# Optimization experiments

Hardware: AMD Instinct MI355X
Metric: run time of the kernel (lower is better)

The kernel has to match this reference:

```python
import jax, jax.numpy as jnp
import numpy as np

N_NODES = 100000


def _sage_conv(x, edge_index, W_l, b_l, W_r):
    # PyG SAGEConv (aggr='mean', root_weight=True):
    #   out = lin_l(mean_{j in N(i)} x_j) + lin_r(x_i)
    src, dst = edge_index[0], edge_index[1]
    msg = x[src]                                            # [E, C] gather
    agg = jax.ops.segment_sum(msg, dst, num_segments=N_NODES)  # [N, C]
    deg = jax.ops.segment_sum(jnp.ones((edge_index.shape[1],), x.dtype), dst,
                              num_segments=N_NODES)
    agg = agg / jnp.maximum(deg, 1.0)[:, None]              # mean aggregation
    return agg @ W_l + b_l + x @ W_r


def setup_inputs() -> dict:
    key = jax.random.key(0)
    ks = jax.random.split(key, 10)
    d, h = 128, 128
    s = 1.0 / np.sqrt(d)
    x = jax.random.normal(ks[0], (N_NODES, d), dtype=jnp.float32)
    edge_index = jax.random.randint(ks[1], (2, 640000), 0, N_NODES, dtype=jnp.int64)
    return {
        "x": x,
        "edge_index": edge_index,
        "W1_l": jax.random.uniform(ks[2], (d, h), jnp.float32, -s, s),
        "b1": jnp.zeros((h,), jnp.float32),
        "W1_r": jax.random.uniform(ks[3], (d, h), jnp.float32, -s, s),
        "W2_l": jax.random.uniform(ks[4], (h, h), jnp.float32, -s, s),
        "b2": jnp.zeros((h,), jnp.float32),
        "W2_r": jax.random.uniform(ks[5], (h, h), jnp.float32, -s, s),
        "W_lin": jax.random.uniform(ks[6], (h, 1), jnp.float32, -s, s),
        "b_lin": jnp.zeros((1,), jnp.float32),
    }


def reference(x, edge_index, W1_l, b1, W1_r, W2_l, b2, W2_r, W_lin, b_lin):
    h = jax.nn.relu(_sage_conv(x, edge_index, W1_l, b1, W1_r))
    h = jax.nn.relu(_sage_conv(h, edge_index, W2_l, b2, W2_r))
    return h @ W_lin + b_lin  # [N, 1]
```

## Files before the change

### kernel.cpp

```cpp
#include <hip/hip_runtime.h>
#include <hip/hip_bf16.h>


#define ND 128
#define KTOT 256
#define CAP 32
#define AGS 136

typedef __bf16 bf16x8 __attribute__((ext_vector_type(8)));
typedef float floatx16 __attribute__((ext_vector_type(16)));

__device__ inline unsigned short f2bf(float f) {
    union { float f; unsigned u; } v; v.f = f;
    unsigned r = v.u + 0x7fffu + ((v.u >> 16) & 1u);
    return (unsigned short)(r >> 16);
}
__device__ inline float bf_lo(unsigned u) { return __uint_as_float(u << 16); }
__device__ inline float bf_hi(unsigned u) { return __uint_as_float(u & 0xffff0000u); }

__device__ inline bf16x8 ldg_bf8(const unsigned short* p, bool ok) {
    int4 v = {0, 0, 0, 0};
    if (ok) v = *(const int4*)p;
    union { int4 i; bf16x8 b; } u; u.i = v;
    return u.b;
}

__global__ void k_prep_all(const float* __restrict__ x, unsigned short* __restrict__ xbf,
                           int nElems,
                           const float* __restrict__ W1l, const float* __restrict__ W1r,
                           unsigned short* __restrict__ Wt1,
                           const float* __restrict__ W2l, const float* __restrict__ W2r,
                           unsigned short* __restrict__ Wt2,
                           const int* __restrict__ esrc_in, const int* __restrict__ edst_in,
                           int* __restrict__ cnt, int* __restrict__ ebuk, int E) {
    const int t = threadIdx.x;
    const int tid = blockIdx.x * 256 + t;

    const int e = blockIdx.x * 128 + t;
    const bool doE = (t < 128) && (e < E);
    int d0 = 0, s0 = 0;
    if (doE) {
        d0 = edst_in[e];
        s0 = esrc_in[e];
    }

    const int i = tid * 8;
    float4 xa, xc;
    const bool doX = (i < nElems);
    if (doX) {
        xa = *(const float4*)(x + i);
        xc = *(const float4*)(x + i + 4);
    }

    int p0 = -1;
    if (doE) p0 = atomicAdd(&cnt[d0], 1);

    if (doX) {
        uint4 r;
        r.x = (unsigned)f2bf(xa.x) | ((unsigned)f2bf(xa.y) << 16);
        r.y = (unsigned)f2bf(xa.z) | ((unsigned)f2bf(xa.w) << 16);
        r.z = (unsigned)f2bf(xc.x) | ((unsigned)f2bf(xc.y) << 16);
        r.w = (unsigned)f2bf(xc.z) | ((unsigned)f2bf(xc.w) << 16);
        *(uint4*)(xbf + i) = r;
    }

    if (tid < 2 * KTOT * ND) {
        const int half = tid >> 15;
        const int idx = tid & 32767;
        const int nn = idx >> 8;
        const int kk = idx & 255;
        const float* Wl = half ? W2l : W1l;
        const float* Wr = half ? W2r : W1r;
        unsigned short* Wt = half ? Wt2 : Wt1;
        float v = (kk < 128) ? Wl[(size_t)kk * ND + nn] : Wr[(size_t)(kk - 128) * ND + nn];
        Wt[(size_t)nn * KTOT + kk] = f2bf(v);
    }

    if (p0 >= 0 && p0 < CAP) ebuk[d0 * CAP + p0] = s0;
}

__device__ __forceinline__ void gather128(const unsigned short* __restrict__ feat,
                                          const int* __restrict__ cnt,
                                          const int* __restrict__ ebuk,
                                          int n, int m0, int t,
                                          unsigned short* Agg) {
    const int l = t & 15;
    const int g = t >> 4;
    for (int p = 0; p < 8; ++p) {
        const int nl = p * 16 + g;
        const int node = m0 + nl;
        int d = 0;
        if (node < n) d = cnt[node];
        const int dd = min(d, CAP);
        const int* lst = ebuk + (size_t)node * CAP;
        float a0 = 0, a1 = 0, a2 = 0, a3 = 0, a4 = 0, a5 = 0, a6 = 0, a7 = 0;
        const int capi = dd - 1;
        for (int j = 0; j < dd; j += 4) {
            int s0 = lst[j];
            int s1 = lst[min(j + 1, capi)];
            int s2 = lst[min(j + 2, capi)];
            int s3 = lst[min(j + 3, capi)];
            uint4 v0 = ((const uint4*)(feat + (size_t)s0 * ND))[l];
            uint4 v1 = ((const uint4*)(feat + (size_t)s1 * ND))[l];
            uint4 v2 = ((const uint4*)(feat + (size_t)s2 * ND))[l];
            uint4 v3 = ((const uint4*)(feat + (size_t)s3 * ND))[l];
            if (j + 1 >= dd) { v1.x = v1.y = v1.z = v1.w = 0u; }
            if (j + 2 >= dd) { v2.x = v2.y = v2.z = v2.w = 0u; }
            if (j + 3 >= dd) { v3.x = v3.y = v3.z = v3.w = 0u; }
            a0 += bf_lo(v0.x) + bf_lo(v1.x) + bf_lo(v2.x) + bf_lo(v3.x);
            a1 += bf_hi(v0.x) + bf_hi(v1.x) + bf_hi(v2.x) + bf_hi(v3.x);
            a2 += bf_lo(v0.y) + bf_lo(v1.y) + bf_lo(v2.y) + bf_lo(v3.y);
            a3 += bf_hi(v0.y) + bf_hi(v1.y) + bf_hi(v2.y) + bf_hi(v3.y);
            a4 += bf_lo(v0.z) + bf_lo(v1.z) + bf_lo(v2.z) + bf_lo(v3.z);
            a5 += bf_hi(v0.z) + bf_hi(v1.z) + bf_hi(v2.z) + bf_hi(v3.z);
            a6 += bf_lo(v0.w) + bf_lo(v1.w) + bf_lo(v2.w) + bf_lo(v3.w);
            a7 += bf_hi(v0.w) + bf_hi(v1.w) + bf_hi(v2.w) + bf_hi(v3.w);
        }
        float inv = 1.0f / (float)max(d, 1);
        uint4 r;
        r.x = (unsigned)f2bf(a0 * inv) | ((unsigned)f2bf(a1 * inv) << 16);
        r.y = (unsigned)f2bf(a2 * inv) | ((unsigned)f2bf(a3 * inv) << 16);
        r.z = (unsigned)f2bf(a4 * inv) | ((unsigned)f2bf(a5 * inv) << 16);
        r.w = (unsigned)f2bf(a6 * inv) | ((unsigned)f2bf(a7 * inv) << 16);
        *(uint4*)&Agg[nl * AGS + l * 8] = r;
    }
}

__launch_bounds__(256, 2)
__global__ void k_layer1_fused(const unsigned short* __restrict__ feat,
                               const unsigned short* __restrict__ Wt,
                               const float* __restrict__ bias,
                               const int* __restrict__ cnt,
                               const int* __restrict__ ebuk,
                               unsigned short* __restrict__ out, int n) {
    __shared__ __align__(16) unsigned short Agg[128 * AGS];
    const int t = threadIdx.x;
    const int m0 = blockIdx.x * 128;

    gather128(feat, cnt, ebuk, n, m0, t, Agg);
    __syncthreads();

    const int wave = t >> 6, lane = t & 63;
    const int l31 = lane & 31, lhalf = lane >> 5;
    const int wm = (wave >> 1) * 64;
    const int wn = (wave & 1) * 64;

    floatx16 acc[2][2];
#pragma unroll
    for (int i = 0; i < 2; ++i)
#pragma unroll
        for (int j = 0; j < 2; ++j) acc[i][j] = (floatx16)0.0f;

#pragma unroll
    for (int kc = 0; kc < 4; ++kc) {
        const int k0 = kc * 32;
        bf16x8 af[2][2], bfr[2][2];
#pragma unroll
        for (int mi = 0; mi < 2; ++mi)
#pragma unroll
            for (int ks = 0; ks < 2; ++ks)
                af[mi][ks] = *(const bf16x8*)&Agg[(wm + mi * 32 + l31) * AGS + k0 + ks * 16 + lhalf * 8];
#pragma unroll
        for (int ni = 0; ni < 2; ++ni)
#pragma unroll
            for (int ks = 0; ks < 2; ++ks)
                bfr[ni][ks] = *(const bf16x8*)(Wt + (size_t)(wn + ni * 32 + l31) * KTOT + k0 + ks * 16 + lhalf * 8);
#pragma unroll
        for (int mi = 0; mi < 2; ++mi)
#pragma unroll
            for (int ni = 0; ni < 2; ++ni) {
                acc[mi][ni] = __builtin_amdgcn_mfma_f32_32x32x16_bf16(af[mi][0], bfr[ni][0], acc[mi][ni], 0, 0, 0);
                acc[mi][ni] = __builtin_amdgcn_mfma_f32_32x32x16_bf16(af[mi][1], bfr[ni][1], acc[mi][ni], 0, 0, 0);
            }
    }

    const int rA0 = m0 + wm + l31;
    const int rA1 = rA0 + 32;
#pragma unroll
    for (int kc = 4; kc < 8; ++kc) {
        const int k0 = kc * 32;
        const int ka = k0 - 128;
        bf16x8 af[2][2], bfr[2][2];
#pragma unroll
        for (int ks = 0; ks < 2; ++ks) {
            af[0][ks] = ldg_bf8(feat + (size_t)rA0 * ND + ka + ks * 16 + lhalf * 8, rA0 < n);
            af[1][ks] = ldg_bf8(feat + (size_t)rA1 * ND + ka + ks * 16 + lhalf * 8, rA1 < n);
        }
#pragma unroll
        for (int ni = 0; ni < 2; ++ni)
#pragma unroll
            for (int ks = 0; ks < 2; ++ks)
                bfr[ni][ks] = *(const bf16x8*)(Wt + (size_t)(wn + ni * 32 + l31) * KTOT + k0 + ks * 16 + lhalf * 8);
#pragma unroll
        for (int mi = 0; mi < 2; ++mi)
#pragma unroll
            for (int ni = 0; ni < 2; ++ni) {
                acc[mi][ni] = __builtin_amdgcn_mfma_f32_32x32x16_bf16(af[mi][0], bfr[ni][0], acc[mi][ni], 0, 0, 0);
                acc[mi][ni] = __builtin_amdgcn_mfma_f32_32x32x16_bf16(af[mi][1], bfr[ni][1], acc[mi][ni], 0, 0, 0);
            }
    }

#pragma unroll
    for (int mi = 0; mi < 2; ++mi)
#pragma unroll
        for (int ni = 0; ni < 2; ++ni) {
            const int c = wn + ni * 32 + l31;
            const float bv = bias[c];
#pragma unroll
            for (int reg = 0; reg < 16; ++reg) {
                const int row = m0 + wm + mi * 32 + lhalf * 4 + (reg & 3) + 8 * (reg >> 2);
                if (row < n) {
                    float v = fmaxf(acc[mi][ni][reg] + bv, 0.f);
                    out[(size_t)row * ND + c] = f2bf(v);
                }
            }
        }
}

__launch_bounds__(256, 2)
__global__ void k_layer2_fused_head(const unsigned short* __restrict__ feat,
                                    const unsigned short* __restrict__ Wt,
                                    const float* __restrict__ bias,
                                    const float* __restrict__ Wlin,
                                    const float* __restrict__ blin,
                                    const int* __restrict__ cnt,
                                    const int* __restrict__ ebuk,
                                    float* __restrict__ out, int n) {
    __shared__ __align__(16) unsigned short Agg[128 * AGS];
    __shared__ float part[128][2];
    const int t = threadIdx.x;
    const int m0 = blockIdx.x * 128;

    gather128(feat, cnt, ebuk, n, m0, t, Agg);
    __syncthreads();

    const int wave = t >> 6, lane = t & 63;
    const int l31 = lane & 31, lhalf = lane >> 5;
    const int wm = (wave >> 1) * 64;
    const int wn = (wave & 1) * 64;

    floatx16 acc[2][2];
#pragma unroll
    for (int i = 0; i < 2; ++i)
#pragma unroll
        for (int j = 0; j < 2; ++j) acc[i][j] = (floatx16)0.0f;

#pragma unroll
    for (int kc = 0; kc < 4; ++kc) {
        const int k0 = kc * 32;
        bf16x8 af[2][2], bfr[2][2];
#pragma unroll
        for (int mi = 0; mi < 2; ++mi)
#pragma unroll
            for (int ks = 0; ks < 2; ++ks)
                af[mi][ks] = *(const bf16x8*)&Agg[(wm + mi * 32 + l31) * AGS + k0 + ks * 16 + lhalf * 8];
#pragma unroll
        for (int ni = 0; ni < 2; ++ni)
#pragma unroll
            for (int ks = 0; ks < 2; ++ks)
                bfr[ni][ks] = *(const bf16x8*)(Wt + (size_t)(wn + ni * 32 + l31) * KTOT + k0 + ks * 16 + lhalf * 8);
#pragma unroll
        for (int mi = 0; mi < 2; ++mi)
#pragma unroll
            for (int ni = 0; ni < 2; ++ni) {
                acc[mi][ni] = __builtin_amdgcn_mfma_f32_32x32x16_bf16(af[mi][0], bfr[ni][0], acc[mi][ni], 0, 0, 0);
                acc[mi][ni] = __builtin_amdgcn_mfma_f32_32x32x16_bf16(af[mi][1], bfr[ni][1], acc[mi][ni], 0, 0, 0);
            }
    }

    const int rA0 = m0 + wm + l31;
    const int rA1 = rA0 + 32;
#pragma unroll
    for (int kc = 4; kc < 8; ++kc) {
        const int k0 = kc * 32;
        const int ka = k0 - 128;
        bf16x8 af[2][2], bfr[2][2];
#pragma unroll
        for (int ks = 0; ks < 2; ++ks) {
            af[0][ks] = ldg_bf8(feat + (size_t)rA0 * ND + ka + ks * 16 + lhalf * 8, rA0 < n);
            af[1][ks] = ldg_bf8(feat + (size_t)rA1 * ND + ka + ks * 16 + lhalf * 8, rA1 < n);
        }
#pragma unroll
        for (int ni = 0; ni < 2; ++ni)
#pragma unroll
            for (int ks = 0; ks < 2; ++ks)
                bfr[ni][ks] = *(const bf16x8*)(Wt + (size_t)(wn + ni * 32 + l31) * KTOT + k0 + ks * 16 + lhalf * 8);
#pragma unroll
        for (int mi = 0; mi < 2; ++mi)
#pragma unroll
            for (int ni = 0; ni < 2; ++ni) {
                acc[mi][ni] = __builtin_amdgcn_mfma_f32_32x32x16_bf16(af[mi][0], bfr[ni][0], acc[mi][ni], 0, 0, 0);
                acc[mi][ni] = __builtin_amdgcn_mfma_f32_32x32x16_bf16(af[mi][1], bfr[ni][1], acc[mi][ni], 0, 0, 0);
            }
    }

#pragma unroll
    for (int mi = 0; mi < 2; ++mi) {
        float p[16];
#pragma unroll
        for (int reg = 0; reg < 16; ++reg) p[reg] = 0.f;
#pragma unroll
        for (int ni = 0; ni < 2; ++ni) {
            const int c = wn + ni * 32 + l31;
            const float bv = bias[c];
            const float wv = Wlin[c];
#pragma unroll
            for (int reg = 0; reg < 16; ++reg) {
                float v = fmaxf(acc[mi][ni][reg] + bv, 0.f);
                p[reg] += v * wv;
            }
        }
#pragma unroll
        for (int reg = 0; reg < 16; ++reg) {
            float v = p[reg];
            v += __shfl_xor(v, 1);
            v += __shfl_xor(v, 2);
            v += __shfl_xor(v, 4);
            v += __shfl_xor(v, 8);
            v += __shfl_xor(v, 16);
            if (l31 == 0) {
                int rl = wm + mi * 32 + lhalf * 4 + (reg & 3) + 8 * (reg >> 2);
                part[rl][wave & 1] = v;
            }
        }
    }
    __syncthreads();
    if (t < 128) {
        int row = m0 + t;
        if (row < n) out[row] = part[t][0] + part[t][1] + blin[0];
    }
}

extern "C" void kernel_launch(void* const* d_in, const int* in_sizes, int n_in,
                              void* d_out, int out_size, void* d_ws, size_t ws_size,
                              hipStream_t stream) {
    const float* x    = (const float*)d_in[0];
    const int*   edge = (const int*)d_in[1];
    const float* W1l  = (const float*)d_in[2];
    const float* b1   = (const float*)d_in[3];
    const float* W1r  = (const float*)d_in[4];
    const float* W2l  = (const float*)d_in[5];
    const float* b2   = (const float*)d_in[6];
    const float* W2r  = (const float*)d_in[7];
    const float* Wlin = (const float*)d_in[8];
    const float* blin = (const float*)d_in[9];
    float* out = (float*)d_out;

    int n = out_size;
    int E = in_sizes[1] / 2;
    (void)n_in; (void)ws_size;

    char* ws = (char*)d_ws;
    size_t off = 0;
    auto take = [&](size_t bytes) -> char* {
        char* p = ws + off;
        off += (bytes + 255) & ~(size_t)255;
        return p;
    };
    int* cnt    = (int*)take((size_t)n * 4);
    int* ebuk   = (int*)take((size_t)n * CAP * 4);
    unsigned short* xbf  = (unsigned short*)take((size_t)n * ND * 2);
    unsigned short* h1bf = (unsigned short*)take((size_t)n * ND * 2);
    unsigned short* Wt1  = (unsigned short*)take((size_t)ND * KTOT * 2);
    unsigned short* Wt2  = (unsigned short*)take((size_t)ND * KTOT * 2);

    hipMemsetAsync(cnt, 0, (size_t)n * 4, stream);

    const int* esrc_in = edge;
    const int* edst_in = edge + E;

    int nElems = n * ND;
    int prepBlocks = (nElems / 8 + 255) / 256;

    k_prep_all<<<prepBlocks, 256, 0, stream>>>(
        x, xbf, nElems, W1l, W1r, Wt1, W2l, W2r, Wt2,
        esrc_in, edst_in, cnt, ebuk, E);

    int gemmBlocks = (n + 127) / 128;

    k_layer1_fused<<<gemmBlocks, 256, 0, stream>>>(xbf, Wt1, b1, cnt, ebuk, h1bf, n);
    k_layer2_fused_head<<<gemmBlocks, 256, 0, stream>>>(h1bf, Wt2, b2, Wlin, blin, cnt, ebuk, out, n);
}
```

Before: 241.7 us.

## Shrink fused SAGE layer row tile to 32 nodes with one MFMA tile per wave

Cuts the rows per block in both fused layer kernels from 128 to 32 and has each of the four waves compute a 32x32 output tile over its own column slice. This gives four times as many blocks with a smaller LDS footprint and fewer accumulator registers, and the launch bound goes from 2 to 4 blocks per SM. The aim is more parallelism and better latency hiding for the irregular neighbor gather, which dominates the runtime. In exchange, the weight matrix is re-read from global memory by four times as many blocks, and the head reduction now sums four partials per row.

```diff
diff --git a/kernel.cpp b/kernel.cpp
--- a/kernel.cpp
+++ b/kernel.cpp
@@ -5,6 +5,7 @@
 #define ND 128
 #define KTOT 256
 #define CAP 32
+#define TM 32
 #define AGS 136
 
 typedef __bf16 bf16x8 __attribute__((ext_vector_type(8)));
@@ -79,14 +80,15 @@
     if (p0 >= 0 && p0 < CAP) ebuk[d0 * CAP + p0] = s0;
 }
 
-__device__ __forceinline__ void gather128(const unsigned short* __restrict__ feat,
-                                          const int* __restrict__ cnt,
-                                          const int* __restrict__ ebuk,
-                                          int n, int m0, int t,
-                                          unsigned short* Agg) {
+__device__ __forceinline__ void gatherTM(const unsigned short* __restrict__ feat,
+                                         const int* __restrict__ cnt,
+                                         const int* __restrict__ ebuk,
+                                         int n, int m0, int t,
+                                         unsigned short* Agg) {
     const int l = t & 15;
     const int g = t >> 4;
-    for (int p = 0; p < 8; ++p) {
+#pragma unroll
+    for (int p = 0; p < TM / 16; ++p) {
         const int nl = p * 16 + g;
         const int node = m0 + nl;
         int d = 0;
@@ -126,98 +128,68 @@
     }
 }
 
-__launch_bounds__(256, 2)
+__launch_bounds__(256, 4)
 __global__ void k_layer1_fused(const unsigned short* __restrict__ feat,
                                const unsigned short* __restrict__ Wt,
                                const float* __restrict__ bias,
                                const int* __restrict__ cnt,
                                const int* __restrict__ ebuk,
                                unsigned short* __restrict__ out, int n) {
-    __shared__ __align__(16) unsigned short Agg[128 * AGS];
+    __shared__ __align__(16) unsigned short Agg[TM * AGS];
     const int t = threadIdx.x;
-    const int m0 = blockIdx.x * 128;
-
-    gather128(feat, cnt, ebuk, n, m0, t, Agg);
+    const int m0 = blockIdx.x * TM;
+
+    gatherTM(feat, cnt, ebuk, n, m0, t, Agg);
     __syncthreads();
 
     const int wave = t >> 6, lane = t & 63;
     const int l31 = lane & 31, lhalf = lane >> 5;
-    const int wm = (wave >> 1) * 64;
-    const int wn = (wave & 1) * 64;
-
-    floatx16 acc[2][2];
-#pragma unroll
-    for (int i = 0; i < 2; ++i)
-#pragma unroll
-        for (int j = 0; j < 2; ++j) acc[i][j] = (floatx16)0.0f;
+    const int wn = wave * 32;
+
+    floatx16 acc = (floatx16)0.0f;
 
 #pragma unroll
     for (int kc = 0; kc < 4; ++kc) {
         const int k0 = kc * 32;
-        bf16x8 af[2][2], bfr[2][2];
-#pragma unroll
-        for (int mi = 0; mi < 2; ++mi)
-#pragma unroll
-            for (int ks = 0; ks < 2; ++ks)
-                af[mi][ks] = *(const bf16x8*)&Agg[(wm + mi * 32 + l31) * AGS + k0 + ks * 16 + lhalf * 8];
-#pragma unroll
-        for (int ni = 0; ni < 2; ++ni)
-#pragma unroll
-            for (int ks = 0; ks < 2; ++ks)
-                bfr[ni][ks] = *(const bf16x8*)(Wt + (size_t)(wn + ni * 32 + l31) * KTOT + k0 + ks * 16 + lhalf * 8);
-#pragma unroll
-        for (int mi = 0; mi < 2; ++mi)
-#pragma unroll
-            for (int ni = 0; ni < 2; ++ni) {
-                acc[mi][ni] = __builtin_amdgcn_mfma_f32_32x32x16_bf16(af[mi][0], bfr[ni][0], acc[mi][ni], 0, 0, 0);
-                acc[mi][ni] = __builtin_amdgcn_mfma_f32_32x32x16_bf16(af[mi][1], bfr[ni][1], acc[mi][ni], 0, 0, 0);
-            }
-    }
-
-    const int rA0 = m0 + wm + l31;
-    const int rA1 = rA0 + 32;
+        bf16x8 af[2], bfr[2];
+#pragma unroll
+        for (int ks = 0; ks < 2; ++ks) {
+            af[ks]  = *(const bf16x8*)&Agg[l31 * AGS + k0 + ks * 16 + lhalf * 8];
+            bfr[ks] = *(const bf16x8*)(Wt + (size_t)(wn + l31) * KTOT + k0 + ks * 16 + lhalf * 8);
+        }
+        acc = __builtin_amdgcn_mfma_f32_32x32x16_bf16(af[0], bfr[0], acc, 0, 0, 0);
+        acc = __builtin_amdgcn_mfma_f32_32x32x16_bf16(af[1], bfr[1], acc, 0, 0, 0);
+    }
+
+    const int rA0 = m0 + l31;
+    const bool okA = rA0 < n;
 #pragma unroll
     for (int kc = 4; kc < 8; ++kc) {
         const int k0 = kc * 32;
         const int ka = k0 - 128;
-        bf16x8 af[2][2], bfr[2][2];
+        bf16x8 af[2], bfr[2];
 #pragma unroll
         for (int ks = 0; ks < 2; ++ks) {
-            af[0][ks] = ldg_bf8(feat + (size_t)rA0 * ND + ka + ks * 16 + lhalf * 8, rA0 < n);
-            af[1][ks] = ldg_bf8(feat + (size_t)rA1 * ND + ka + ks * 16 + lhalf * 8, rA1 < n);
-        }
-#pragma unroll
-        for (int ni = 0; ni < 2; ++ni)
-#pragma unroll
-            for (int ks = 0; ks < 2; ++ks)
-                bfr[ni][ks] = *(const bf16x8*)(Wt + (size_t)(wn + ni * 32 + l31) * KTOT + k0 + ks * 16 + lhalf * 8);
-#pragma unroll
-        for (int mi = 0; mi < 2; ++mi)
-#pragma unroll
-            for (int ni = 0; ni < 2; ++ni) {
-                acc[mi][ni] = __builtin_amdgcn_mfma_f32_32x32x16_bf16(af[mi][0], bfr[ni][0], acc[mi][ni], 0, 0, 0);
-                acc[mi][ni] = __builtin_amdgcn_mfma_f32_32x32x16_bf16(af[mi][1], bfr[ni][1], acc[mi][ni], 0, 0, 0);
-            }
-    }
-
-#pragma unroll
-    for (int mi = 0; mi < 2; ++mi)
-#pragma unroll
-        for (int ni = 0; ni < 2; ++ni) {
-            const int c = wn + ni * 32 + l31;
-            const float bv = bias[c];
-#pragma unroll
-            for (int reg = 0; reg < 16; ++reg) {
-                const int row = m0 + wm + mi * 32 + lhalf * 4 + (reg & 3) + 8 * (reg >> 2);
-                if (row < n) {
-                    float v = fmaxf(acc[mi][ni][reg] + bv, 0.f);
-                    out[(size_t)row * ND + c] = f2bf(v);
-                }
-            }
-        }
-}
-
-__launch_bounds__(256, 2)
+            af[ks]  = ldg_bf8(feat + (size_t)rA0 * ND + ka + ks * 16 + lhalf * 8, okA);
+            bfr[ks] = *(const bf16x8*)(Wt + (size_t)(wn + l31) * KTOT + k0 + ks * 16 + lhalf * 8);
+        }
+        acc = __builtin_amdgcn_mfma_f32_32x32x16_bf16(af[0], bfr[0], acc, 0, 0, 0);
+        acc = __builtin_amdgcn_mfma_f32_32x32x16_bf16(af[1], bfr[1], acc, 0, 0, 0);
+    }
+
+    const int c = wn + l31;
+    const float bv = bias[c];
+#pragma unroll
+    for (int reg = 0; reg < 16; ++reg) {
+        const int row = m0 + lhalf * 4 + (reg & 3) + 8 * (reg >> 2);
+        if (row < n) {
+            float v = fmaxf(acc[reg] + bv, 0.f);
+            out[(size_t)row * ND + c] = f2bf(v);
+        }
+    }
+}
+
+__launch_bounds__(256, 4)
 __global__ void k_layer2_fused_head(const unsigned short* __restrict__ feat,
                                     const unsigned short* __restrict__ Wt,
                                     const float* __restrict__ bias,
@@ -226,108 +198,74 @@
                                     const int* __restrict__ cnt,
                                     const int* __restrict__ ebuk,
                                     float* __restrict__ out, int n) {
-    __shared__ __align__(16) unsigned short Agg[128 * AGS];
-    __shared__ float part[128][2];
+    __shared__ __align__(16) unsigned short Agg[TM * AGS];
+    __shared__ float part[TM][4];
     const int t = threadIdx.x;
-    const int m0 = blockIdx.x * 128;
-
-    gather128(feat, cnt, ebuk, n, m0, t, Agg);
+    const int m0 = blockIdx.x * TM;
+
+    gatherTM(feat, cnt, ebuk, n, m0, t, Agg);
     __syncthreads();
 
     const int wave = t >> 6, lane = t & 63;
     const int l31 = lane & 31, lhalf = lane >> 5;
-    const int wm = (wave >> 1) * 64;
-    const int wn = (wave & 1) * 64;
-
-    floatx16 acc[2][2];
-#pragma unroll
-    for (int i = 0; i < 2; ++i)
-#pragma unroll
-        for (int j = 0; j < 2; ++j) acc[i][j] = (floatx16)0.0f;
+    const int wn = wave * 32;
+
+    floatx16 acc = (floatx16)0.0f;
 
 #pragma unroll
     for (int kc = 0; kc < 4; ++kc) {
         const int k0 = kc * 32;
-        bf16x8 af[2][2], bfr[2][2];
-#pragma unroll
-        for (int mi = 0; mi < 2; ++mi)
-#pragma unroll
-            for (int ks = 0; ks < 2; ++ks)
-                af[mi][ks] = *(const bf16x8*)&Agg[(wm + mi * 32 + l31) * AGS + k0 + ks * 16 + lhalf * 8];
-#pragma unroll
-        for (int ni = 0; ni < 2; ++ni)
-#pragma unroll
-            for (int ks = 0; ks < 2; ++ks)
-                bfr[ni][ks] = *(const bf16x8*)(Wt + (size_t)(wn + ni * 32 + l31) * KTOT + k0 + ks * 16 + lhalf * 8);
-#pragma unroll
-        for (int mi = 0; mi < 2; ++mi)
-#pragma unroll
-            for (int ni = 0; ni < 2; ++ni) {
-                acc[mi][ni] = __builtin_amdgcn_mfma_f32_32x32x16_bf16(af[mi][0], bfr[ni][0], acc[mi][ni], 0, 0, 0);
-                acc[mi][ni] = __builtin_amdgcn_mfma_f32_32x32x16_bf16(af[mi][1], bfr[ni][1], acc[mi][ni], 0, 0, 0);
-            }
-    }
-
-    const int rA0 = m0 + wm + l31;
-    const int rA1 = rA0 + 32;
+        bf16x8 af[2], bfr[2];
+#pragma unroll
+        for (int ks = 0; ks < 2; ++ks) {
+            af[ks]  = *(const bf16x8*)&Agg[l31 * AGS + k0 + ks * 16 + lhalf * 8];
+            bfr[ks] = *(const bf16x8*)(Wt + (size_t)(wn + l31) * KTOT + k0 + ks * 16 + lhalf * 8);
+        }
+        acc = __builtin_amdgcn_mfma_f32_32x32x16_bf16(af[0], bfr[0], acc, 0, 0, 0);
+        acc = __builtin_amdgcn_mfma_f32_32x32x16_bf16(af[1], bfr[1], acc, 0, 0, 0);
+    }
+
+    const int rA0 = m0 + l31;
+    const bool okA = rA0 < n;
 #pragma unroll
     for (int kc = 4; kc < 8; ++kc) {
         const int k0 = kc * 32;
         const int ka = k0 - 128;
-        bf16x8 af[2][2], bfr[2][2];
+        bf16x8 af[2], bfr[2];
 #pragma unroll
         for (int ks = 0; ks < 2; ++ks) {
-            af[0][ks] = ldg_bf8(feat + (size_t)rA0 * ND + ka + ks * 16 + lhalf * 8, rA0 < n);
-            af[1][ks] = ldg_bf8(feat + (size_t)rA1 * ND + ka + ks * 16 + lhalf * 8, rA1 < n);
-        }
-#pragma unroll
-        for (int ni = 0; ni < 2; ++ni)
-#pragma unroll
-            for (int ks = 0; ks < 2; ++ks)
-                bfr[ni][ks] = *(const bf16x8*)(Wt + (size_t)(wn + ni * 32 + l31) * KTOT + k0 + ks * 16 + lhalf * 8);
-#pragma unroll
-        for (int mi = 0; mi < 2; ++mi)
-#pragma unroll
-            for (int ni = 0; ni < 2; ++ni) {
-                acc[mi][ni] = __builtin_amdgcn_mfma_f32_32x32x16_bf16(af[mi][0], bfr[ni][0], acc[mi][ni], 0, 0, 0);
-                acc[mi][ni] = __builtin_amdgcn_mfma_f32_32x32x16_bf16(af[mi][1], bfr[ni][1], acc[mi][ni], 0, 0, 0);
-            }
-    }
-
-#pragma unroll
-    for (int mi = 0; mi < 2; ++mi) {
-        float p[16];
-#pragma unroll
-        for (int reg = 0; reg < 16; ++reg) p[reg] = 0.f;
-#pragma unroll
-        for (int ni = 0; ni < 2; ++ni) {
-            const int c = wn + ni * 32 + l31;
-            const float bv = bias[c];
-            const float wv = Wlin[c];
-#pragma unroll
-            for (int reg = 0; reg < 16; ++reg) {
-                float v = fmaxf(acc[mi][ni][reg] + bv, 0.f);
-                p[reg] += v * wv;
-            }
-        }
-#pragma unroll
-        for (int reg = 0; reg < 16; ++reg) {
-            float v = p[reg];
-            v += __shfl_xor(v, 1);
-            v += __shfl_xor(v, 2);
-            v += __shfl_xor(v, 4);
-            v += __shfl_xor(v, 8);
-            v += __shfl_xor(v, 16);
-            if (l31 == 0) {
-                int rl = wm + mi * 32 + lhalf * 4 + (reg & 3) + 8 * (reg >> 2);
-                part[rl][wave & 1] = v;
-            }
+            af[ks]  = ldg_bf8(feat + (size_t)rA0 * ND + ka + ks * 16 + lhalf * 8, okA);
+            bfr[ks] = *(const bf16x8*)(Wt + (size_t)(wn + l31) * KTOT + k0 + ks * 16 + lhalf * 8);
+        }
+        acc = __builtin_amdgcn_mfma_f32_32x32x16_bf16(af[0], bfr[0], acc, 0, 0, 0);
+        acc = __builtin_amdgcn_mfma_f32_32x32x16_bf16(af[1], bfr[1], acc, 0, 0, 0);
+    }
+
+    const int c = wn + l31;
+    const float bv = bias[c];
+    const float wv = Wlin[c];
+    float p[16];
+#pragma unroll
+    for (int reg = 0; reg < 16; ++reg)
+        p[reg] = fmaxf(acc[reg] + bv, 0.f) * wv;
+#pragma unroll
+    for (int reg = 0; reg < 16; ++reg) {
+        float v = p[reg];
+        v += __shfl_xor(v, 1);
+        v += __shfl_xor(v, 2);
+        v += __shfl_xor(v, 4);
+        v += __shfl_xor(v, 8);
+        v += __shfl_xor(v, 16);
+        if (l31 == 0) {
+            int rl = lhalf * 4 + (reg & 3) + 8 * (reg >> 2);
+            part[rl][wave] = v;
         }
     }
     __syncthreads();
-    if (t < 128) {
+    if (t < TM) {
         int row = m0 + t;
-        if (row < n) out[row] = part[t][0] + part[t][1] + blin[0];
+        if (row < n)
+            out[row] = part[t][0] + part[t][1] + part[t][2] + part[t][3] + blin[0];
     }
 }
 
@@ -376,7 +314,7 @@
         x, xbf, nElems, W1l, W1r, Wt1, W2l, W2r, Wt2,
         esrc_in, edst_in, cnt, ebuk, E);
 
-    int gemmBlocks = (n + 127) / 128;
+    int gemmBlocks = (n + TM - 1) / TM;
 
     k_layer1_fused<<<gemmBlocks, 256, 0, stream>>>(xbf, Wt1, b1, cnt, ebuk, h1bf, n);
     k_layer2_fused_head<<<gemmBlocks, 256, 0, stream>>>(h1bf, Wt2, b2, Wlin, blin, cnt, ebuk, out, n);
```

Measured after the change: 250.3 us. +3.5%, slower.
